# Kernel optimization log

Measured on AMD Instinct MI355X. Metric: run time of the kernel, lower is better.

## Reference

```python
import jax, jax.numpy as jnp
import numpy as np

B, T, D, H = 2, 2048, 1024, 16
HS = D // H  # per-head size = head_size//num_heads with head_size=D
EPS = 1e-5


def layer_norm(x, g, b):
    mu = jnp.mean(x, axis=-1, keepdims=True)
    var = jnp.mean((x - mu) ** 2, axis=-1, keepdims=True)
    return (x - mu) * jax.lax.rsqrt(var + EPS) * g + b


def setup_inputs() -> dict:
    key = jax.random.key(0)
    ks = jax.random.split(key, 12)
    s = lambda n: 1.0 / np.sqrt(n)
    return {
        "x": jax.random.normal(ks[0], (B, T, D), dtype=jnp.float32),
        "Wq": jax.random.normal(ks[1], (H, D, HS), dtype=jnp.float32) * s(D),
        "Wk": jax.random.normal(ks[2], (H, D, HS), dtype=jnp.float32) * s(D),
        "Wv": jax.random.normal(ks[3], (H, D, HS), dtype=jnp.float32) * s(D),
        "Wproj": jax.random.normal(ks[4], (D, D), dtype=jnp.float32) * s(D),
        "bproj": jnp.zeros((D,), dtype=jnp.float32),
        "W1": jax.random.normal(ks[5], (D, 4 * D), dtype=jnp.float32) * s(D),
        "b1": jnp.zeros((4 * D,), dtype=jnp.float32),
        "W2": jax.random.normal(ks[6], (4 * D, D), dtype=jnp.float32) * s(4 * D),
        "b2": jnp.zeros((D,), dtype=jnp.float32),
        "ln1_g": jnp.ones((D,), dtype=jnp.float32),
        "ln1_b": jnp.zeros((D,), dtype=jnp.float32),
        "ln2_g": jnp.ones((D,), dtype=jnp.float32),
        "ln2_b": jnp.zeros((D,), dtype=jnp.float32),
    }


def reference(x, Wq, Wk, Wv, Wproj, bproj, W1, b1, W2, b2, ln1_g, ln1_b, ln2_g, ln2_b):
    # x = LN1(x); x = x + sa(x)  (residual uses normalized x, per source)
    xn = layer_norm(x, ln1_g, ln1_b)
    q = jnp.einsum("btd,hde->bhte", xn, Wq)  # [B,H,T,HS]
    k = jnp.einsum("btd,hde->bhte", xn, Wk)
    v = jnp.einsum("btd,hde->bhte", xn, Wv)
    # scale uses C = embedding dim (not head size), per source
    scores = jnp.einsum("bhqe,bhke->bhqk", q, k) * (D ** -0.5)
    mask = jnp.tril(jnp.ones((T, T), dtype=bool))  # [Tq,Tk]
    scores = jnp.where(mask, scores, -jnp.inf)
    # softmax over dim=1 of [B,T,T] in source => QUERY axis (axis=2 here)
    w = jax.nn.softmax(scores, axis=2)
    attn = jnp.einsum("bhqk,bhke->bhqe", w, v)  # [B,H,T,HS]
    attn = attn.transpose(0, 2, 1, 3).reshape(B, T, D)
    sa = attn @ Wproj + bproj
    x1 = xn + sa
    # x = LN2(x); x = x + ffwd(x)
    x1n = layer_norm(x1, ln2_g, ln2_b)
    h = jax.nn.relu(x1n @ W1 + b1)
    ff = h @ W2 + b2
    return x1n + ff
```

## Files before the change

### kernel.cpp

```cpp
#include <hip/hip_runtime.h>
#include <math.h>

#define B_ 2
#define T_ 2048
#define D_ 1024
#define H_ 16
#define HS_ 64
#define BT_ (B_*T_)
#define EPS_ 1e-5f
#define SCALE_ 0.03125f
#define C2_ (0.03125f * 1.44269504088896f)

typedef __attribute__((ext_vector_type(4))) float f32x4;
typedef __attribute__((ext_vector_type(8))) __bf16 bf16x8;

__device__ __forceinline__ short f2bf(float f) {
    union { float f; unsigned u; } cv; cv.f = f;
    unsigned u = cv.u;
    return (short)((u + 0x7fffu + ((u >> 16) & 1u)) >> 16);
}

__global__ __launch_bounds__(256) void ln_kernel(const float* __restrict__ x,
        const float* __restrict__ g, const float* __restrict__ b,
        float* __restrict__ out, short* __restrict__ outb) {
    int row = blockIdx.x;
    int tid = threadIdx.x;
    const float* xr = x + (size_t)row * D_;
    float4 v = *(const float4*)(xr + tid * 4);
    __shared__ float red[256];
    red[tid] = v.x + v.y + v.z + v.w;
    __syncthreads();
    for (int st = 128; st > 0; st >>= 1) {
        if (tid < st) red[tid] += red[tid + st];
        __syncthreads();
    }
    float mean = red[0] * (1.0f / D_);
    __syncthreads();
    float dx = v.x - mean, dy = v.y - mean, dz = v.z - mean, dw = v.w - mean;
    red[tid] = dx*dx + dy*dy + dz*dz + dw*dw;
    __syncthreads();
    for (int st = 128; st > 0; st >>= 1) {
        if (tid < st) red[tid] += red[tid + st];
        __syncthreads();
    }
    float rstd = rsqrtf(red[0] * (1.0f / D_) + EPS_);
    float4 gv = *(const float4*)(g + tid * 4);
    float4 bv = *(const float4*)(b + tid * 4);
    float4 o;
    o.x = dx * rstd * gv.x + bv.x;
    o.y = dy * rstd * gv.y + bv.y;
    o.z = dz * rstd * gv.z + bv.z;
    o.w = dw * rstd * gv.w + bv.w;
    *(float4*)(out + (size_t)row * D_ + tid * 4) = o;
    short4 ob = make_short4(f2bf(o.x), f2bf(o.y), f2bf(o.z), f2bf(o.w));
    *(short4*)(outb + (size_t)row * D_ + tid * 4) = ob;
}

__global__ __launch_bounds__(256) void transpose_cvt(const float* __restrict__ in,
        short* __restrict__ out, int R, int C) {
    __shared__ float t[32][33];
    int c0 = blockIdx.x * 32, r0 = blockIdx.y * 32;
    const float* inb = in + (size_t)blockIdx.z * R * C;
    short* outb = out + (size_t)blockIdx.z * R * C;
    int tx = threadIdx.x & 31, ty = threadIdx.x >> 5;
    #pragma unroll
    for (int i = 0; i < 32; i += 8)
        t[ty + i][tx] = inb[(size_t)(r0 + ty + i) * C + c0 + tx];
    __syncthreads();
    #pragma unroll
    for (int i = 0; i < 32; i += 8)
        outb[(size_t)(c0 + ty + i) * R + r0 + tx] = f2bf(t[tx][ty + i]);
}

__global__ __launch_bounds__(256) void gemm_qkv(
        const short* __restrict__ A, const short* __restrict__ Bt,
        short* __restrict__ qo, short* __restrict__ ko, short* __restrict__ vo,
        int M, int N, int K) {
    __shared__ char As[2][16384];
    __shared__ char Bs[2][8192];
    int tid = threadIdx.x, lane = tid & 63, w = tid >> 6;

    int orig = blockIdx.y * gridDim.x + blockIdx.x;
    int cpx = (gridDim.x * gridDim.y) >> 3;
    int wgid = (orig & 7) * cpx + (orig >> 3);
    int m0 = (wgid / gridDim.x) * 128;
    int n0 = (wgid % gridDim.x) * 64;

    const size_t Kb = (size_t)K * 2;
    int rowA[4], cbA[4], rowB[2], cbB[2];
    #pragma unroll
    for (int i = 0; i < 4; ++i) {
        int o = (w * 4 + i) * 1024 + lane * 16;
        rowA[i] = o >> 7;
        cbA[i] = (o & 127) ^ ((rowA[i] & 7) << 4);
    }
    #pragma unroll
    for (int i = 0; i < 2; ++i) {
        int o = (w * 2 + i) * 1024 + lane * 16;
        rowB[i] = o >> 7;
        cbB[i] = (o & 127) ^ ((rowB[i] & 7) << 4);
    }

    #define STAGE_Q(buf, kt) do {                                              \
        _Pragma("unroll")                                                      \
        for (int i_ = 0; i_ < 4; ++i_) {                                       \
            const char* ga_ = (const char*)A + (size_t)(m0 + rowA[i_]) * Kb    \
                              + (size_t)(kt) * 2 + cbA[i_];                    \
            __builtin_amdgcn_global_load_lds(                                  \
                (const __attribute__((address_space(1))) void*)ga_,            \
                (__attribute__((address_space(3))) void*)(As[buf] + (w * 4 + i_) * 1024),\
                16, 0, 0);                                                     \
        }                                                                      \
        _Pragma("unroll")                                                      \
        for (int i_ = 0; i_ < 2; ++i_) {                                       \
            const char* gb_ = (const char*)Bt + (size_t)(n0 + rowB[i_]) * Kb   \
                              + (size_t)(kt) * 2 + cbB[i_];                    \
            __builtin_amdgcn_global_load_lds(                                  \
                (const __attribute__((address_space(1))) void*)gb_,            \
                (__attribute__((address_space(3))) void*)(Bs[buf] + (w * 2 + i_) * 1024),\
                16, 0, 0);                                                     \
        }                                                                      \
    } while (0)

    f32x4 acc[2][4] = {};
    int nt = K >> 6;
    STAGE_Q(0, 0);
    for (int t = 0; t < nt; ++t) {
        int cur = t & 1;
        if (t + 1 < nt) {
            STAGE_Q(cur ^ 1, (t + 1) * 64);
            asm volatile("s_waitcnt vmcnt(6)" ::: "memory");
        } else {
            asm volatile("s_waitcnt vmcnt(0)" ::: "memory");
        }
        __builtin_amdgcn_s_barrier();
        __builtin_amdgcn_s_setprio(1);
        #pragma unroll
        for (int kk = 0; kk < 2; ++kk) {
            int kbyte = kk * 64 + (lane >> 4) * 16;
            bf16x8 bf[4], af[2];
            #pragma unroll
            for (int ni = 0; ni < 4; ++ni) {
                int row = ni * 16 + (lane & 15);
                bf[ni] = *(const bf16x8*)(Bs[cur] + row * 128 + (kbyte ^ ((row & 7) << 4)));
            }
            #pragma unroll
            for (int mi = 0; mi < 2; ++mi) {
                int row = w * 32 + mi * 16 + (lane & 15);
                af[mi] = *(const bf16x8*)(As[cur] + row * 128 + (kbyte ^ ((row & 7) << 4)));
            }
            #pragma unroll
            for (int mi = 0; mi < 2; ++mi)
                #pragma unroll
                for (int ni = 0; ni < 4; ++ni)
                    acc[mi][ni] = __builtin_amdgcn_mfma_f32_16x16x32_bf16(
                        af[mi], bf[ni], acc[mi][ni], 0, 0, 0);
        }
        __builtin_amdgcn_s_setprio(0);
        __builtin_amdgcn_s_barrier();
    }
    #undef STAGE_Q

    int sel = n0 >> 10, hh = (n0 & 1023) >> 6;
    #pragma unroll
    for (int mi = 0; mi < 2; ++mi) {
        #pragma unroll
        for (int j = 0; j < 4; ++j) {
            int row = m0 + w * 32 + mi * 16 + (lane >> 4) * 4 + j;
            int bb = row >> 11, tt = row & 2047;
            #pragma unroll
            for (int ni = 0; ni < 4; ++ni) {
                int e = ni * 16 + (lane & 15);
                short bv = f2bf(acc[mi][ni][j]);
                if (sel == 0)
                    qo[(((size_t)(bb * H_ + hh)) * T_ + tt) * HS_ + e] = bv;
                else if (sel == 1)
                    ko[(((size_t)(bb * H_ + hh)) * T_ + tt) * HS_ + e] = bv;
                else
                    vo[(((size_t)(bb * H_ + hh)) * HS_ + e) * T_ + tt] = bv;
            }
        }
    }
}

__global__ __launch_bounds__(256) void gemm128_sk(
        const short* __restrict__ A, const short* __restrict__ Bt,
        float* __restrict__ P, int M, int N, int Ksl, int Ktot) {
    __shared__ char As[2][16384];
    __shared__ char Bs[2][16384];
    int tid = threadIdx.x;
    int lane = tid & 63, w = tid >> 6;
    int wr = w >> 1, wc = w & 1;

    int orig = blockIdx.y * gridDim.x + blockIdx.x;
    int cpx = (gridDim.x * gridDim.y) >> 3;
    int wgid = (orig & 7) * cpx + (orig >> 3);
    int m0 = (wgid / gridDim.x) * 128;
    int n0 = (wgid % gridDim.x) * 128;
    int k0 = blockIdx.z * Ksl;
    float* Pz = P + (size_t)blockIdx.z * M * N;

    f32x4 acc[4][4] = {};

    int rowS[4], kbS[4];
    #pragma unroll
    for (int i = 0; i < 4; ++i) {
        int o = (w * 4 + i) * 1024 + lane * 16;
        rowS[i] = o >> 7;
        kbS[i] = (o & 127) ^ ((rowS[i] & 7) << 4);
    }
    const size_t Kb = (size_t)Ktot * 2;

    #define STAGE_K(buf, kt) do {                                              \
        _Pragma("unroll")                                                      \
        for (int i_ = 0; i_ < 4; ++i_) {                                       \
            int c_ = w * 4 + i_;                                               \
            const char* ga_ = (const char*)A + (size_t)(m0 + rowS[i_]) * Kb    \
                              + (size_t)(k0 + (kt)) * 2 + kbS[i_];             \
            __builtin_amdgcn_global_load_lds(                                  \
                (const __attribute__((address_space(1))) void*)ga_,            \
                (__attribute__((address_space(3))) void*)(As[buf] + c_ * 1024),\
                16, 0, 0);                                                     \
            const char* gb_ = (const char*)Bt + (size_t)(n0 + rowS[i_]) * Kb   \
                              + (size_t)(k0 + (kt)) * 2 + kbS[i_];             \
            __builtin_amdgcn_global_load_lds(                                  \
                (const __attribute__((address_space(1))) void*)gb_,            \
                (__attribute__((address_space(3))) void*)(Bs[buf] + c_ * 1024),\
                16, 0, 0);                                                     \
        }                                                                      \
    } while (0)

    int nt = Ksl >> 6;
    STAGE_K(0, 0);
    for (int t = 0; t < nt; ++t) {
        int cur = t & 1;
        if (t + 1 < nt) {
            STAGE_K(cur ^ 1, (t + 1) * 64);
            asm volatile("s_waitcnt vmcnt(8)" ::: "memory");
        } else {
            asm volatile("s_waitcnt vmcnt(0)" ::: "memory");
        }
        __builtin_amdgcn_s_barrier();
        __builtin_amdgcn_s_setprio(1);
        #pragma unroll
        for (int kk = 0; kk < 2; ++kk) {
            int kbyte = kk * 64 + (lane >> 4) * 16;
            bf16x8 af[4], bf[4];
            #pragma unroll
            for (int mi = 0; mi < 4; ++mi) {
                int row = wr * 64 + mi * 16 + (lane & 15);
                af[mi] = *(const bf16x8*)(As[cur] + row * 128 + (kbyte ^ ((row & 7) << 4)));
            }
            #pragma unroll
            for (int ni = 0; ni < 4; ++ni) {
                int row = wc * 64 + ni * 16 + (lane & 15);
                bf[ni] = *(const bf16x8*)(Bs[cur] + row * 128 + (kbyte ^ ((row & 7) << 4)));
            }
            #pragma unroll
            for (int mi = 0; mi < 4; ++mi)
                #pragma unroll
                for (int ni = 0; ni < 4; ++ni)
                    acc[mi][ni] = __builtin_amdgcn_mfma_f32_16x16x32_bf16(
                        af[mi], bf[ni], acc[mi][ni], 0, 0, 0);
        }
        __builtin_amdgcn_s_setprio(0);
        __builtin_amdgcn_s_barrier();
    }
    #undef STAGE_K

    #pragma unroll
    for (int mi = 0; mi < 4; ++mi) {
        #pragma unroll
        for (int j = 0; j < 4; ++j) {
            int row = m0 + wr * 64 + mi * 16 + (lane >> 4) * 4 + j;
            #pragma unroll
            for (int ni = 0; ni < 4; ++ni) {
                int col = n0 + wc * 64 + ni * 16 + (lane & 15);
                Pz[(size_t)row * N + col] = acc[mi][ni][j];
            }
        }
    }
}

__global__ __launch_bounds__(256) void addreduce(const float* __restrict__ p0,
        const float* __restrict__ p1, const float* __restrict__ bias,
        const float* __restrict__ res, float* __restrict__ out) {
    int i = blockIdx.x * 256 + threadIdx.x;
    float4 a = ((const float4*)p0)[i];
    float4 b = ((const float4*)p1)[i];
    float4 r = ((const float4*)res)[i];
    float4 bs = ((const float4*)bias)[i & 255];
    float4 o;
    o.x = a.x + b.x + r.x + bs.x;
    o.y = a.y + b.y + r.y + bs.y;
    o.z = a.z + b.z + r.z + bs.z;
    o.w = a.w + b.w + r.w + bs.w;
    ((float4*)out)[i] = o;
}

template<bool BIAS, bool RES, bool RELU, bool BF16OUT>
__global__ __launch_bounds__(256) void gemm_12864(
        const short* __restrict__ A, const short* __restrict__ Bt,
        const float* __restrict__ bias, const float* __restrict__ res,
        float* __restrict__ C, short* __restrict__ Cb,
        int M, int N, int K) {
    __shared__ char As[2][16384];
    __shared__ char Bs[2][8192];
    int tid = threadIdx.x, lane = tid & 63, w = tid >> 6;

    int orig = blockIdx.y * gridDim.x + blockIdx.x;
    int cpx = (gridDim.x * gridDim.y) >> 3;
    int wgid = (orig & 7) * cpx + (orig >> 3);
    int m0 = (wgid / gridDim.x) * 128;
    int n0 = (wgid % gridDim.x) * 64;

    const size_t Kb = (size_t)K * 2;
    int rowA[4], cbA[4], rowB[2], cbB[2];
    #pragma unroll
    for (int i = 0; i < 4; ++i) {
        int o = (w * 4 + i) * 1024 + lane * 16;
        rowA[i] = o >> 7;
        cbA[i] = (o & 127) ^ ((rowA[i] & 7) << 4);
    }
    #pragma unroll
    for (int i = 0; i < 2; ++i) {
        int o = (w * 2 + i) * 1024 + lane * 16;
        rowB[i] = o >> 7;
        cbB[i] = (o & 127) ^ ((rowB[i] & 7) << 4);
    }

    #define STAGE_S(buf, kt) do {                                              \
        _Pragma("unroll")                                                      \
        for (int i_ = 0; i_ < 4; ++i_) {                                       \
            const char* ga_ = (const char*)A + (size_t)(m0 + rowA[i_]) * Kb    \
                              + (size_t)(kt) * 2 + cbA[i_];                    \
            __builtin_amdgcn_global_load_lds(                                  \
                (const __attribute__((address_space(1))) void*)ga_,            \
                (__attribute__((address_space(3))) void*)(As[buf] + (w * 4 + i_) * 1024),\
                16, 0, 0);                                                     \
        }                                                                      \
        _Pragma("unroll")                                                      \
        for (int i_ = 0; i_ < 2; ++i_) {                                       \
            const char* gb_ = (const char*)Bt + (size_t)(n0 + rowB[i_]) * Kb   \
                              + (size_t)(kt) * 2 + cbB[i_];                    \
            __builtin_amdgcn_global_load_lds(                                  \
                (const __attribute__((address_space(1))) void*)gb_,            \
                (__attribute__((address_space(3))) void*)(Bs[buf] + (w * 2 + i_) * 1024),\
                16, 0, 0);                                                     \
        }                                                                      \
    } while (0)

    f32x4 acc[2][4] = {};
    int nt = K >> 6;
    STAGE_S(0, 0);
    for (int t = 0; t < nt; ++t) {
        int cur = t & 1;
        if (t + 1 < nt) {
            STAGE_S(cur ^ 1, (t + 1) * 64);
            asm volatile("s_waitcnt vmcnt(6)" ::: "memory");
        } else {
            asm volatile("s_waitcnt vmcnt(0)" ::: "memory");
        }
        __builtin_amdgcn_s_barrier();
        __builtin_amdgcn_s_setprio(1);
        #pragma unroll
        for (int kk = 0; kk < 2; ++kk) {
            int kbyte = kk * 64 + (lane >> 4) * 16;
            bf16x8 bf[4], af[2];
            #pragma unroll
            for (int ni = 0; ni < 4; ++ni) {
                int row = ni * 16 + (lane & 15);
                bf[ni] = *(const bf16x8*)(Bs[cur] + row * 128 + (kbyte ^ ((row & 7) << 4)));
            }
            #pragma unroll
            for (int mi = 0; mi < 2; ++mi) {
                int row = w * 32 + mi * 16 + (lane & 15);
                af[mi] = *(const bf16x8*)(As[cur] + row * 128 + (kbyte ^ ((row & 7) << 4)));
            }
            #pragma unroll
            for (int mi = 0; mi < 2; ++mi)
                #pragma unroll
                for (int ni = 0; ni < 4; ++ni)
                    acc[mi][ni] = __builtin_amdgcn_mfma_f32_16x16x32_bf16(
                        af[mi], bf[ni], acc[mi][ni], 0, 0, 0);
        }
        __builtin_amdgcn_s_setprio(0);
        __builtin_amdgcn_s_barrier();
    }
    #undef STAGE_S

    #pragma unroll
    for (int mi = 0; mi < 2; ++mi) {
        #pragma unroll
        for (int j = 0; j < 4; ++j) {
            int row = m0 + w * 32 + mi * 16 + (lane >> 4) * 4 + j;
            #pragma unroll
            for (int ni = 0; ni < 4; ++ni) {
                int col = n0 + ni * 16 + (lane & 15);
                float vv = acc[mi][ni][j];
                if (BIAS) vv += bias[col];
                if (RES)  vv += res[(size_t)row * N + col];
                if (RELU) vv = fmaxf(vv, 0.0f);
                if (BF16OUT) Cb[(size_t)row * N + col] = f2bf(vv);
                else         C[(size_t)row * N + col] = vv;
            }
        }
    }
}

template<bool BIAS, bool RELU, bool BF16OUT>
__global__ __launch_bounds__(512, 2) void gemm256_2p(
        const short* __restrict__ A, const short* __restrict__ Bt,
        const float* __restrict__ bias,
        float* __restrict__ C, short* __restrict__ Cb,
        int M, int N, int K) {
    __shared__ char As[2][32768];
    __shared__ char Bs[2][32768];
    int tid = threadIdx.x, lane = tid & 63, w = tid >> 6;
    int wr = w >> 2, wc = w & 3;

    int nwg = gridDim.x * gridDim.y;
    int orig = blockIdx.y * gridDim.x + blockIdx.x;
    int cpx = nwg >> 3;
    int wgid = (orig & 7) * cpx + (orig >> 3);
    int m0 = (wgid / gridDim.x) * 256;
    int n0 = (wgid % gridDim.x) * 256;

    const size_t Kb = (size_t)K * 2;
    int rowS[4], cbS[4];
    #pragma unroll
    for (int i = 0; i < 4; ++i) {
        int o = (i * 8 + w) * 1024 + lane * 16;
        rowS[i] = o >> 7;
        cbS[i] = (o & 127) ^ ((rowS[i] & 7) << 4);
    }

    #define STAGE_256(buf, kt) do {                                           \
        _Pragma("unroll")                                                     \
        for (int i_ = 0; i_ < 4; ++i_) {                                      \
            int c_ = i_ * 8 + w;                                              \
            const char* ga_ = (const char*)A + (size_t)(m0 + rowS[i_]) * Kb   \
                              + (size_t)(kt) * 2 + cbS[i_];                   \
            __builtin_amdgcn_global_load_lds(                                 \
                (const __attribute__((address_space(1))) void*)ga_,           \
                (__attribute__((address_space(3))) void*)(As[buf] + c_ * 1024),\
                16, 0, 0);                                                    \
            const char* gb_ = (const char*)Bt + (size_t)(n0 + rowS[i_]) * Kb  \
                              + (size_t)(kt) * 2 + cbS[i_];                   \
            __builtin_amdgcn_global_load_lds(                                 \
                (const __attribute__((address_space(1))) void*)gb_,           \
                (__attribute__((address_space(3))) void*)(Bs[buf] + c_ * 1024),\
                16, 0, 0);                                                    \
        }                                                                     \
    } while (0)

    f32x4 acc[8][4] = {};
    int nt = K >> 6;
    STAGE_256(0, 0);
    for (int t = 0; t < nt; ++t) {
        int cur = t & 1;
        if (t + 1 < nt) {
            STAGE_256(cur ^ 1, (t + 1) * 64);
            asm volatile("s_waitcnt vmcnt(8)" ::: "memory");
        } else {
            asm volatile("s_waitcnt vmcnt(0)" ::: "memory");
        }
        __builtin_amdgcn_s_barrier();
        __builtin_amdgcn_s_setprio(1);
        #pragma unroll
        for (int kk = 0; kk < 2; ++kk) {
            int kbyte = kk * 64 + (lane >> 4) * 16;
            bf16x8 bfr[4];
            #pragma unroll
            for (int ni = 0; ni < 4; ++ni) {
                int row = wc * 64 + ni * 16 + (lane & 15);
                bfr[ni] = *(const bf16x8*)(Bs[cur] + row * 128 + (kbyte ^ ((row & 7) << 4)));
            }
            #pragma unroll
            for (int mi = 0; mi < 8; ++mi) {
                int row = wr * 128 + mi * 16 + (lane & 15);
                bf16x8 afr = *(const bf16x8*)(As[cur] + row * 128 + (kbyte ^ ((row & 7) << 4)));
                #pragma unroll
                for (int ni = 0; ni < 4; ++ni)
                    acc[mi][ni] = __builtin_amdgcn_mfma_f32_16x16x32_bf16(
                        afr, bfr[ni], acc[mi][ni], 0, 0, 0);
            }
        }
        __builtin_amdgcn_s_setprio(0);
        __builtin_amdgcn_s_barrier();
    }
    #undef STAGE_256

    #pragma unroll
    for (int mi = 0; mi < 8; ++mi) {
        #pragma unroll
        for (int j = 0; j < 4; ++j) {
            int row = m0 + wr * 128 + mi * 16 + (lane >> 4) * 4 + j;
            #pragma unroll
            for (int ni = 0; ni < 4; ++ni) {
                int col = n0 + wc * 64 + ni * 16 + (lane & 15);
                float vv = acc[mi][ni][j];
                if (BIAS) vv += bias[col];
                if (RELU) vv = fmaxf(vv, 0.0f);
                if (BF16OUT) Cb[(size_t)row * N + col] = f2bf(vv);
                else         C[(size_t)row * N + col] = vv;
            }
        }
    }
}

__global__ __launch_bounds__(256) void attn_pass1_mfma(
        const short* __restrict__ qg, const short* __restrict__ kg,
        float* __restrict__ lpart) {
    int orig = (blockIdx.z * 4 + blockIdx.y) * 16 + blockIdx.x;
    int wgid = (orig & 7) * 256 + (orig >> 3);
    int kt = wgid & 15;
    int chunk = (wgid >> 4) & 3;
    int bh = wgid >> 6;
    int tid = threadIdx.x, lane = tid & 63, w = tid >> 6;
    __shared__ char Qs[8192];
    const size_t base = (size_t)bh * T_ * HS_;
    int kb0 = kt * 128;
    bf16x8 af[2][2];
    #pragma unroll
    for (int s2 = 0; s2 < 2; ++s2) {
        const short* kr = kg + base
            + (size_t)(kb0 + s2 * 64 + w * 16 + (lane & 15)) * HS_ + (lane >> 4) * 8;
        af[s2][0] = *(const bf16x8*)kr;
        af[s2][1] = *(const bf16x8*)(kr + 32);
    }
    int baseT = kt * 2;
    int R = 32 - baseT;
    int cnt = (R + 3) >> 2;
    int qs = baseT + chunk * cnt;
    int qe = qs + cnt; if (qe > 32) qe = 32;
    float psum[2][4] = {};
    for (int qt = qs; qt < qe; ++qt) {
        __syncthreads();
        #pragma unroll
        for (int it = 0; it < 2; ++it) {
            int o = it * 4096 + w * 1024 + lane * 16;
            int row = o >> 7;
            int col = (o & 127) ^ ((row & 7) << 4);
            const char* src = (const char*)(qg + base + (size_t)(qt * 64 + row) * HS_) + col;
            __builtin_amdgcn_global_load_lds(
                (const __attribute__((address_space(1))) void*)src,
                (__attribute__((address_space(3))) void*)(Qs + it * 4096 + w * 1024), 16, 0, 0);
        }
        __syncthreads();
        bool anymask = (qt < baseT + 2);
        #pragma unroll
        for (int sub = 0; sub < 4; ++sub) {
            int qrow = sub * 16 + (lane & 15);
            bf16x8 bq[2];
            #pragma unroll
            for (int kk = 0; kk < 2; ++kk) {
                int off = (kk * 64 + (lane >> 4) * 16) ^ ((qrow & 7) << 4);
                bq[kk] = *(const bf16x8*)(Qs + qrow * 128 + off);
            }
            int qglob = qt * 64 + qrow;
            #pragma unroll
            for (int s2 = 0; s2 < 2; ++s2) {
                f32x4 c = {0.f, 0.f, 0.f, 0.f};
                c = __builtin_amdgcn_mfma_f32_16x16x32_bf16(af[s2][0], bq[0], c, 0, 0, 0);
                c = __builtin_amdgcn_mfma_f32_16x16x32_bf16(af[s2][1], bq[1], c, 0, 0, 0);
                if (anymask) {
                    #pragma unroll
                    for (int j = 0; j < 4; ++j) {
                        int kglob = kb0 + s2 * 64 + w * 16 + (lane >> 4) * 4 + j;
                        float pe = exp2f(c[j] * C2_);
                        psum[s2][j] += (qglob >= kglob) ? pe : 0.0f;
                    }
                } else {
                    #pragma unroll
                    for (int j = 0; j < 4; ++j)
                        psum[s2][j] += exp2f(c[j] * C2_);
                }
            }
        }
    }
    #pragma unroll
    for (int s2 = 0; s2 < 2; ++s2)
        #pragma unroll
        for (int j = 0; j < 4; ++j) {
            float v = psum[s2][j];
            v += __shfl_xor(v, 1); v += __shfl_xor(v, 2);
            v += __shfl_xor(v, 4); v += __shfl_xor(v, 8);
            psum[s2][j] = v;
        }
    if ((lane & 15) == 0) {
        #pragma unroll
        for (int s2 = 0; s2 < 2; ++s2)
            #pragma unroll
            for (int j = 0; j < 4; ++j)
                lpart[((size_t)chunk * 32 + bh) * T_
                      + kb0 + s2 * 64 + w * 16 + (lane >> 4) * 4 + j] = psum[s2][j];
    }
}

__global__ __launch_bounds__(256) void lreduce(const float* __restrict__ lpart,
        float* __restrict__ rl) {
    int i = blockIdx.x * 256 + threadIdx.x;
    const int S = 32 * T_;
    float s = lpart[i] + lpart[S + i] + lpart[2 * S + i] + lpart[3 * S + i];
    rl[i] = -log2f(s);
}

__global__ __launch_bounds__(256) void attn_pass2_mfma(
        const short* __restrict__ qg, const short* __restrict__ kg,
        const short* __restrict__ vt, const float* __restrict__ rl,
        short* __restrict__ attnb) {
    int orig = blockIdx.y * 16 + blockIdx.x;
    int wgid = (orig & 7) * 64 + (orig >> 3);
    int pair = wgid & 15;
    int bh = wgid >> 4;
    int bb = bh >> 4, hh = bh & 15;
    int tid = threadIdx.x, lane = tid & 63, w = tid >> 6;
    __shared__ char Kb[2][8192];
    __shared__ char Vb[2][8192];
    __shared__ char Ps[8192];
    __shared__ float rlAll[2048];
    const size_t qkbase = (size_t)bh * T_ * HS_;
    const size_t vtbase = (size_t)bh * HS_ * T_;

    {
        const float4* rp = (const float4*)(rl + (size_t)bh * T_);
        #pragma unroll
        for (int i = 0; i < 2; ++i)
            *(float4*)&rlAll[(tid * 2 + i) * 4] = rp[tid * 2 + i];
    }
    __syncthreads();

    #pragma unroll 1
    for (int half = 0; half < 2; ++half) {
        int qtile = half == 0 ? pair : 31 - pair;
        int q0 = qtile * 64 + w * 16;
        bf16x8 aq[2];
        {
            const short* qr = qg + qkbase + (size_t)(q0 + (lane & 15)) * HS_ + (lane >> 4) * 8;
            aq[0] = *(const bf16x8*)qr;
            aq[1] = *(const bf16x8*)(qr + 32);
        }
        f32x4 oacc[4] = {};
        int nstep = qtile + 1;

        #define STAGE64(bufi, stepi) do {                                         \
            int k0_ = (stepi) * 64;                                               \
            _Pragma("unroll")                                                     \
            for (int i_ = 0; i_ < 2; ++i_) {                                      \
                int c_ = w * 2 + i_;                                              \
                int o_ = c_ * 1024 + lane * 16;                                   \
                int row_ = o_ >> 7;                                               \
                int col_ = (o_ & 127) ^ ((row_ & 7) << 4);                        \
                const char* srcK_ = (const char*)(kg + qkbase                     \
                    + (size_t)(k0_ + row_) * HS_) + col_;                         \
                __builtin_amdgcn_global_load_lds(                                 \
                    (const __attribute__((address_space(1))) void*)srcK_,         \
                    (__attribute__((address_space(3))) void*)(Kb[bufi] + c_ * 1024), \
                    16, 0, 0);                                                    \
                const char* srcV_ = (const char*)(vt + vtbase                     \
                    + (size_t)row_ * T_ + k0_) + col_;                            \
                __builtin_amdgcn_global_load_lds(                                 \
                    (const __attribute__((address_space(1))) void*)srcV_,         \
                    (__attribute__((address_space(3))) void*)(Vb[bufi] + c_ * 1024), \
                    16, 0, 0);                                                    \
            }                                                                     \
        } while (0)

        STAGE64(0, 0);
        for (int st = 0; st < nstep; ++st) {
            int cur = st & 1;
            if (st + 1 < nstep) {
                STAGE64(cur ^ 1, st + 1);
                asm volatile("s_waitcnt vmcnt(4)" ::: "memory");
            } else {
                asm volatile("s_waitcnt vmcnt(0)" ::: "memory");
            }
            __builtin_amdgcn_s_barrier();
            int kbase = st * 64;
            bool diag = (st == qtile);
            int qgl = q0 + (lane & 15);
            int ql = w * 16 + (lane & 15);
            int swz = (ql & 7) << 4;
            #pragma unroll
            for (int sub = 0; sub < 4; ++sub) {
                int krow = sub * 16 + (lane & 15);
                f32x4 c = {0.f, 0.f, 0.f, 0.f};
                #pragma unroll
                for (int kk = 0; kk < 2; ++kk) {
                    int off = (kk * 64 + (lane >> 4) * 16) ^ ((krow & 7) << 4);
                    bf16x8 bk = *(const bf16x8*)(Kb[cur] + krow * 128 + off);
                    c = __builtin_amdgcn_mfma_f32_16x16x32_bf16(bk, aq[kk], c, 0, 0, 0);
                }
                int kloc0 = sub * 16 + (lane >> 4) * 4;
                f32x4 lg4 = *(const f32x4*)&rlAll[kbase + kloc0];
                float wv[4];
                if (!diag) {
                    #pragma unroll
                    for (int j = 0; j < 4; ++j)
                        wv[j] = exp2f(fmaf(c[j], C2_, lg4[j]));
                } else {
                    #pragma unroll
                    for (int j = 0; j < 4; ++j) {
                        float t = exp2f(fmaf(c[j], C2_, lg4[j]));
                        int keyg = kbase + kloc0 + j;
                        wv[j] = (qgl < keyg) ? 0.0f : t;
                    }
                }
                unsigned p01, p23;
                asm("v_cvt_pk_bf16_f32 %0, %1, %2" : "=v"(p01) : "v"(wv[0]), "v"(wv[1]));
                asm("v_cvt_pk_bf16_f32 %0, %1, %2" : "=v"(p23) : "v"(wv[2]), "v"(wv[3]));
                *(unsigned*)(Ps + ql * 128 + ((kloc0 * 2) ^ swz)) = p01;
                *(unsigned*)(Ps + ql * 128 + ((kloc0 * 2 + 4) ^ swz)) = p23;
            }
            bf16x8 ap[2];
            #pragma unroll
            for (int kk = 0; kk < 2; ++kk) {
                int off = (kk * 64 + (lane >> 4) * 16) ^ swz;
                ap[kk] = *(const bf16x8*)(Ps + ql * 128 + off);
            }
            __builtin_amdgcn_s_setprio(1);
            #pragma unroll
            for (int es = 0; es < 4; ++es) {
                int erow = es * 16 + (lane & 15);
                #pragma unroll
                for (int kk = 0; kk < 2; ++kk) {
                    int vcol = (kk * 64 + (lane >> 4) * 16) ^ ((erow & 7) << 4);
                    bf16x8 bv = *(const bf16x8*)(Vb[cur] + erow * 128 + vcol);
                    oacc[es] = __builtin_amdgcn_mfma_f32_16x16x32_bf16(
                        ap[kk], bv, oacc[es], 0, 0, 0);
                }
            }
            __builtin_amdgcn_s_setprio(0);
            __builtin_amdgcn_s_barrier();
        }
        #undef STAGE64
        #pragma unroll
        for (int es = 0; es < 4; ++es) {
            #pragma unroll
            for (int j = 0; j < 4; ++j) {
                int qgl = q0 + (lane >> 4) * 4 + j;
                int e = es * 16 + (lane & 15);
                attnb[((size_t)(bb * T_ + qgl)) * D_ + hh * HS_ + e] = f2bf(oacc[es][j]);
            }
        }
    }
}

extern "C" void kernel_launch(void* const* d_in, const int* in_sizes, int n_in,
                              void* d_out, int out_size, void* d_ws, size_t ws_size,
                              hipStream_t stream) {
    const float* x     = (const float*)d_in[0];
    const float* Wq    = (const float*)d_in[1];
    const float* Wk    = (const float*)d_in[2];
    const float* Wv    = (const float*)d_in[3];
    const float* Wproj = (const float*)d_in[4];
    const float* bproj = (const float*)d_in[5];
    const float* W1    = (const float*)d_in[6];
    const float* b1    = (const float*)d_in[7];
    const float* W2    = (const float*)d_in[8];
    const float* b2    = (const float*)d_in[9];
    const float* ln1g  = (const float*)d_in[10];
    const float* ln1b  = (const float*)d_in[11];
    const float* ln2g  = (const float*)d_in[12];
    const float* ln2b  = (const float*)d_in[13];
    float* out = (float*)d_out;

    const size_t MB = 1u << 20;
    char* ws = (char*)d_ws;
    float* xn    = (float*)(ws + 0 * MB);
    short* xnb   = (short*)(ws + 16 * MB);
    short* qbh   = (short*)(ws + 24 * MB);
    short* kbh   = (short*)(ws + 32 * MB);
    short* vtb   = (short*)(ws + 40 * MB);
    short* attnb = (short*)(ws + 48 * MB);
    float* x1    = (float*)(ws + 56 * MB);
    float* x1n   = (float*)(ws + 72 * MB);
    short* x1nb  = (short*)(ws + 88 * MB);
    short* hb    = (short*)(ws + 96 * MB);
    short* wqkv  = (short*)(ws + 128 * MB);
    short* wprjt = (short*)(ws + 134 * MB);
    short* w1t   = (short*)(ws + 136 * MB);
    short* w2t   = (short*)(ws + 144 * MB);
    float* lpart = (float*)(ws + 152 * MB);
    float* rl    = (float*)(ws + 153 * MB);
    float* partP = (float*)(ws + 0 * MB);
    float* part0 = (float*)(ws + 0 * MB);
    float* part1 = (float*)(ws + 16 * MB);

    transpose_cvt<<<dim3(2, 32, 16), 256, 0, stream>>>(Wq, wqkv + (size_t)0 * 1048576, 1024, 64);
    transpose_cvt<<<dim3(2, 32, 16), 256, 0, stream>>>(Wk, wqkv + (size_t)1 * 1048576, 1024, 64);
    transpose_cvt<<<dim3(2, 32, 16), 256, 0, stream>>>(Wv, wqkv + (size_t)2 * 1048576, 1024, 64);
    transpose_cvt<<<dim3(32, 32, 1), 256, 0, stream>>>(Wproj, wprjt, 1024, 1024);
    transpose_cvt<<<dim3(128, 32, 1), 256, 0, stream>>>(W1, w1t, 1024, 4096);
    transpose_cvt<<<dim3(32, 128, 1), 256, 0, stream>>>(W2, w2t, 4096, 1024);

    ln_kernel<<<dim3(BT_), 256, 0, stream>>>(x, ln1g, ln1b, xn, xnb);
    gemm_qkv<<<dim3(48, 32), 256, 0, stream>>>(
        xnb, wqkv, qbh, kbh, vtb, BT_, 3072, 1024);
    attn_pass1_mfma<<<dim3(16, 4, 32), 256, 0, stream>>>(qbh, kbh, lpart);
    lreduce<<<dim3(32 * T_ / 256), 256, 0, stream>>>(lpart, rl);
    attn_pass2_mfma<<<dim3(16, 32), 256, 0, stream>>>(qbh, kbh, vtb, rl, attnb);
    gemm_12864<true, true, false, false><<<dim3(16, 32), 256, 0, stream>>>(
        attnb, wprjt, bproj, xn, x1, nullptr, BT_, 1024, 1024);
    ln_kernel<<<dim3(BT_), 256, 0, stream>>>(x1, ln2g, ln2b, x1n, x1nb);
    gemm256_2p<true, true, true><<<dim3(16, 16), 512, 0, stream>>>(
        x1nb, w1t, b1, nullptr, hb, BT_, 4096, 1024);
    gemm128_sk<<<dim3(8, 32, 2), 256, 0, stream>>>(
        hb, w2t, partP, BT_, 1024, 2048, 4096);
    addreduce<<<dim3(BT_ * D_ / 4 / 256), 256, 0, stream>>>(
        part0, part1, b2, x1n, out);
    (void)in_sizes; (void)n_in; (void)out_size; (void)ws_size;
}
```

Measured before the change: 278.4 us.

## Drop fp32 LN outputs, use bf16 residuals, and merge weight transposes into one launch

The layer-norm kernel now writes only a bf16 copy, and the projection epilogue and final add read the residual from that bf16 buffer instead of an fp32 one. This removes two fp32 writes and their later reads. The six weight transpose-and-convert launches are also combined into one flat-grid kernel to cut launch overhead. The cost is lower residual precision, since the residual path now carries bf16 rounding error into the output.

```diff
diff --git a/kernel.cpp b/kernel.cpp
--- a/kernel.cpp
+++ b/kernel.cpp
@@ -19,10 +19,15 @@
     unsigned u = cv.u;
     return (short)((u + 0x7fffu + ((u >> 16) & 1u)) >> 16);
 }
+__device__ __forceinline__ float bf2f(short s) {
+    union { unsigned u; float f; } cv;
+    cv.u = ((unsigned)(unsigned short)s) << 16;
+    return cv.f;
+}
 
 __global__ __launch_bounds__(256) void ln_kernel(const float* __restrict__ x,
         const float* __restrict__ g, const float* __restrict__ b,
-        float* __restrict__ out, short* __restrict__ outb) {
+        short* __restrict__ outb) {
     int row = blockIdx.x;
     int tid = threadIdx.x;
     const float* xr = x + (size_t)row * D_;
@@ -46,30 +51,51 @@
     float rstd = rsqrtf(red[0] * (1.0f / D_) + EPS_);
     float4 gv = *(const float4*)(g + tid * 4);
     float4 bv = *(const float4*)(b + tid * 4);
-    float4 o;
-    o.x = dx * rstd * gv.x + bv.x;
-    o.y = dy * rstd * gv.y + bv.y;
-    o.z = dz * rstd * gv.z + bv.z;
-    o.w = dw * rstd * gv.w + bv.w;
-    *(float4*)(out + (size_t)row * D_ + tid * 4) = o;
-    short4 ob = make_short4(f2bf(o.x), f2bf(o.y), f2bf(o.z), f2bf(o.w));
+    short4 ob = make_short4(
+        f2bf(dx * rstd * gv.x + bv.x),
+        f2bf(dy * rstd * gv.y + bv.y),
+        f2bf(dz * rstd * gv.z + bv.z),
+        f2bf(dw * rstd * gv.w + bv.w));
     *(short4*)(outb + (size_t)row * D_ + tid * 4) = ob;
 }
 
-__global__ __launch_bounds__(256) void transpose_cvt(const float* __restrict__ in,
-        short* __restrict__ out, int R, int C) {
+__global__ __launch_bounds__(256) void transpose_all(
+        const float* __restrict__ Wq, const float* __restrict__ Wk,
+        const float* __restrict__ Wv, const float* __restrict__ Wproj,
+        const float* __restrict__ W1, const float* __restrict__ W2,
+        short* __restrict__ wqkv, short* __restrict__ wprjt,
+        short* __restrict__ w1t, short* __restrict__ w2t) {
+    int flat = blockIdx.x;
+    const float* in; short* out; int R, C, c0, r0;
+    if (flat < 3072) {
+        int job = flat >> 10, rem = flat & 1023;
+        const float* src = job == 0 ? Wq : (job == 1 ? Wk : Wv);
+        in  = src + (size_t)(rem >> 6) * 65536;
+        out = wqkv + (size_t)job * 1048576 + (size_t)(rem >> 6) * 65536;
+        R = 1024; C = 64;
+        c0 = (rem & 1) * 32; r0 = ((rem >> 1) & 31) * 32;
+    } else if (flat < 4096) {
+        int rem = flat - 3072;
+        in = Wproj; out = wprjt; R = 1024; C = 1024;
+        c0 = (rem & 31) * 32; r0 = (rem >> 5) * 32;
+    } else if (flat < 8192) {
+        int rem = flat - 4096;
+        in = W1; out = w1t; R = 1024; C = 4096;
+        c0 = (rem & 127) * 32; r0 = (rem >> 7) * 32;
+    } else {
+        int rem = flat - 8192;
+        in = W2; out = w2t; R = 4096; C = 1024;
+        c0 = (rem & 31) * 32; r0 = (rem >> 5) * 32;
+    }
     __shared__ float t[32][33];
-    int c0 = blockIdx.x * 32, r0 = blockIdx.y * 32;
-    const float* inb = in + (size_t)blockIdx.z * R * C;
-    short* outb = out + (size_t)blockIdx.z * R * C;
     int tx = threadIdx.x & 31, ty = threadIdx.x >> 5;
     #pragma unroll
     for (int i = 0; i < 32; i += 8)
-        t[ty + i][tx] = inb[(size_t)(r0 + ty + i) * C + c0 + tx];
+        t[ty + i][tx] = in[(size_t)(r0 + ty + i) * C + c0 + tx];
     __syncthreads();
     #pragma unroll
     for (int i = 0; i < 32; i += 8)
-        outb[(size_t)(c0 + ty + i) * R + r0 + tx] = f2bf(t[tx][ty + i]);
+        out[(size_t)(c0 + ty + i) * R + r0 + tx] = f2bf(t[tx][ty + i]);
 }
 
 __global__ __launch_bounds__(256) void gemm_qkv(
@@ -284,24 +310,24 @@
 
 __global__ __launch_bounds__(256) void addreduce(const float* __restrict__ p0,
         const float* __restrict__ p1, const float* __restrict__ bias,
-        const float* __restrict__ res, float* __restrict__ out) {
+        const short* __restrict__ resb, float* __restrict__ out) {
     int i = blockIdx.x * 256 + threadIdx.x;
     float4 a = ((const float4*)p0)[i];
     float4 b = ((const float4*)p1)[i];
-    float4 r = ((const float4*)res)[i];
+    short4 rs = ((const short4*)resb)[i];
     float4 bs = ((const float4*)bias)[i & 255];
     float4 o;
-    o.x = a.x + b.x + r.x + bs.x;
-    o.y = a.y + b.y + r.y + bs.y;
-    o.z = a.z + b.z + r.z + bs.z;
-    o.w = a.w + b.w + r.w + bs.w;
+    o.x = a.x + b.x + bf2f(rs.x) + bs.x;
+    o.y = a.y + b.y + bf2f(rs.y) + bs.y;
+    o.z = a.z + b.z + bf2f(rs.z) + bs.z;
+    o.w = a.w + b.w + bf2f(rs.w) + bs.w;
     ((float4*)out)[i] = o;
 }
 
 template<bool BIAS, bool RES, bool RELU, bool BF16OUT>
 __global__ __launch_bounds__(256) void gemm_12864(
         const short* __restrict__ A, const short* __restrict__ Bt,
-        const float* __restrict__ bias, const float* __restrict__ res,
+        const float* __restrict__ bias, const short* __restrict__ resb,
         float* __restrict__ C, short* __restrict__ Cb,
         int M, int N, int K) {
     __shared__ char As[2][16384];
@@ -399,7 +425,7 @@
                 int col = n0 + ni * 16 + (lane & 15);
                 float vv = acc[mi][ni][j];
                 if (BIAS) vv += bias[col];
-                if (RES)  vv += res[(size_t)row * N + col];
+                if (RES)  vv += bf2f(resb[(size_t)row * N + col]);
                 if (RELU) vv = fmaxf(vv, 0.0f);
                 if (BF16OUT) Cb[(size_t)row * N + col] = f2bf(vv);
                 else         C[(size_t)row * N + col] = vv;
@@ -768,14 +794,12 @@
 
     const size_t MB = 1u << 20;
     char* ws = (char*)d_ws;
-    float* xn    = (float*)(ws + 0 * MB);
     short* xnb   = (short*)(ws + 16 * MB);
     short* qbh   = (short*)(ws + 24 * MB);
     short* kbh   = (short*)(ws + 32 * MB);
     short* vtb   = (short*)(ws + 40 * MB);
     short* attnb = (short*)(ws + 48 * MB);
     float* x1    = (float*)(ws + 56 * MB);
-    float* x1n   = (float*)(ws + 72 * MB);
     short* x1nb  = (short*)(ws + 88 * MB);
     short* hb    = (short*)(ws + 96 * MB);
     short* wqkv  = (short*)(ws + 128 * MB);
@@ -788,27 +812,23 @@
     float* part0 = (float*)(ws + 0 * MB);
     float* part1 = (float*)(ws + 16 * MB);
 
-    transpose_cvt<<<dim3(2, 32, 16), 256, 0, stream>>>(Wq, wqkv + (size_t)0 * 1048576, 1024, 64);
-    transpose_cvt<<<dim3(2, 32, 16), 256, 0, stream>>>(Wk, wqkv + (size_t)1 * 1048576, 1024, 64);
-    transpose_cvt<<<dim3(2, 32, 16), 256, 0, stream>>>(Wv, wqkv + (size_t)2 * 1048576, 1024, 64);
-    transpose_cvt<<<dim3(32, 32, 1), 256, 0, stream>>>(Wproj, wprjt, 1024, 1024);
-    transpose_cvt<<<dim3(128, 32, 1), 256, 0, stream>>>(W1, w1t, 1024, 4096);
-    transpose_cvt<<<dim3(32, 128, 1), 256, 0, stream>>>(W2, w2t, 4096, 1024);
-
-    ln_kernel<<<dim3(BT_), 256, 0, stream>>>(x, ln1g, ln1b, xn, xnb);
+    transpose_all<<<dim3(12288), 256, 0, stream>>>(
+        Wq, Wk, Wv, Wproj, W1, W2, wqkv, wprjt, w1t, w2t);
+
+    ln_kernel<<<dim3(BT_), 256, 0, stream>>>(x, ln1g, ln1b, xnb);
     gemm_qkv<<<dim3(48, 32), 256, 0, stream>>>(
         xnb, wqkv, qbh, kbh, vtb, BT_, 3072, 1024);
     attn_pass1_mfma<<<dim3(16, 4, 32), 256, 0, stream>>>(qbh, kbh, lpart);
     lreduce<<<dim3(32 * T_ / 256), 256, 0, stream>>>(lpart, rl);
     attn_pass2_mfma<<<dim3(16, 32), 256, 0, stream>>>(qbh, kbh, vtb, rl, attnb);
     gemm_12864<true, true, false, false><<<dim3(16, 32), 256, 0, stream>>>(
-        attnb, wprjt, bproj, xn, x1, nullptr, BT_, 1024, 1024);
-    ln_kernel<<<dim3(BT_), 256, 0, stream>>>(x1, ln2g, ln2b, x1n, x1nb);
+        attnb, wprjt, bproj, xnb, x1, nullptr, BT_, 1024, 1024);
+    ln_kernel<<<dim3(BT_), 256, 0, stream>>>(x1, ln2g, ln2b, x1nb);
     gemm256_2p<true, true, true><<<dim3(16, 16), 512, 0, stream>>>(
         x1nb, w1t, b1, nullptr, hb, BT_, 4096, 1024);
     gemm128_sk<<<dim3(8, 32, 2), 256, 0, stream>>>(
         hb, w2t, partP, BT_, 1024, 2048, 4096);
     addreduce<<<dim3(BT_ * D_ / 4 / 256), 256, 0, stream>>>(
-        part0, part1, b2, x1n, out);
+        part0, part1, b2, x1nb, out);
     (void)in_sizes; (void)n_in; (void)out_size; (void)ws_size;
 }
```

New measurement: 264.4 us, median of 3. 5.0% less time.
